# Kernel tuning notes

Hardware: AMD Instinct MI355X
Metric: run time of the kernel (lower is better)

The kernel has to match this reference:

```python
import jax, jax.numpy as jnp
import numpy as np
import math

B, T, C, H = 2, 2048, 1024, 16
D = C // H  # head dim 64

def setup_inputs() -> dict:
    key = jax.random.key(0)
    ks = jax.random.split(key, 3)
    scale = 0.02
    return {
        "x": jax.random.normal(ks[0], (B, T, C), dtype=jnp.float32),
        "W_attn": jax.random.normal(ks[1], (C, 3 * C), dtype=jnp.float32) * scale,
        "b_attn": jnp.zeros((3 * C,), dtype=jnp.float32),
        "W_proj": jax.random.normal(ks[2], (C, C), dtype=jnp.float32) * scale,
        "b_proj": jnp.zeros((C,), dtype=jnp.float32),
    }

def reference(x, W_attn, b_attn, W_proj, b_proj):
    Bb, Tt, Cc = x.shape
    qkv = x @ W_attn + b_attn                       # [B,T,3C]
    q, k, v = jnp.split(qkv, 3, axis=-1)
    # [B,T,C] -> [B,H,T,D]
    def heads(t):
        return t.reshape(Bb, Tt, H, D).transpose(0, 2, 1, 3)
    q, k, v = heads(q), heads(k), heads(v)
    scores = jnp.einsum('bhqd,bhkd->bhqk', q, k) * (1.0 / math.sqrt(D))
    causal = jnp.tril(jnp.ones((Tt, Tt), dtype=bool))
    scores = jnp.where(causal, scores, -jnp.inf)
    attn = jax.nn.softmax(scores, axis=-1)
    out = jnp.einsum('bhqk,bhkd->bhqd', attn, v)    # [B,H,T,D]
    out = out.transpose(0, 2, 1, 3).reshape(Bb, Tt, Cc)
    return out @ W_proj + b_proj
```

## Files before the change

kernel.cpp:

```cpp
#include <hip/hip_runtime.h>

typedef unsigned short u16;
typedef unsigned int u32;
typedef float f32x4 __attribute__((ext_vector_type(4)));
typedef float f32x16 __attribute__((ext_vector_type(16)));
typedef unsigned int u32x4 __attribute__((ext_vector_type(4)));
typedef unsigned int u32x2 __attribute__((ext_vector_type(2)));
typedef unsigned short u16x8 __attribute__((ext_vector_type(8)));
typedef unsigned short u16x4 __attribute__((ext_vector_type(4)));

#define DEV static __device__ __forceinline__

constexpr int BB = 2, TT = 2048, CC = 1024, HH = 16, DD = 64;
constexpr int MDIM = BB * TT;

DEV u16 f2bf(float f) {
  unsigned int u = __builtin_bit_cast(unsigned int, f);
  u += 0x7fffu + ((u >> 16) & 1u);
  return (u16)(u >> 16);
}
DEV float bf2f(u16 h) {
  unsigned int u = ((unsigned int)h) << 16;
  return __builtin_bit_cast(float, u);
}
DEV void async16(const void* g, void* l) {
  __builtin_amdgcn_global_load_lds(
      (const __attribute__((address_space(1))) unsigned int*)g,
      (__attribute__((address_space(3))) unsigned int*)l, 16, 0, 0);
}
DEV void mfma16(f32x4& acc, u32x4 a, u32x4 b) {
  asm volatile("v_mfma_f32_16x16x32_bf16 %0, %1, %2, %0"
               : "+v"(acc)
               : "v"(a), "v"(b));
}
DEV void mfma32(f32x16& acc, u32x4 a, u32x4 b) {
  asm volatile("v_mfma_f32_32x32x16_bf16 %0, %1, %2, %0"
               : "+v"(acc)
               : "v"(a), "v"(b));
}
DEV u32 cvtpk(float lo, float hi) {
  u32 r;
  asm("v_cvt_pk_bf16_f32 %0, %1, %2" : "=v"(r) : "v"(lo), "v"(hi));
  return r;
}
DEV void pswap(u32& a, u32& b) {
#if __has_builtin(__builtin_amdgcn_permlane32_swap)
  u32x2 r = __builtin_amdgcn_permlane32_swap(a, b, false, false);
  a = r.x;
  b = r.y;
#else
  asm volatile("v_permlane32_swap_b32 %0, %1" : "+v"(a), "+v"(b));
#endif
}
DEV float exp2g(float x) {
#if __has_builtin(__builtin_amdgcn_exp2f)
  return __builtin_amdgcn_exp2f(x);
#else
  return exp2f(x);
#endif
}

__global__ void cvt_f32_bf16(const float* __restrict__ in, u16* __restrict__ out, int n) {
  const int i = (blockIdx.x * blockDim.x + threadIdx.x) * 4;
  if (i < n) {
    f32x4 v = *(const f32x4*)(in + i);
    u16x4 o;
#pragma unroll
    for (int j = 0; j < 4; ++j) o[j] = f2bf(v[j]);
    *(u16x4*)(out + i) = o;
  }
}

__global__ void transpose_both(const float* __restrict__ Wa, const float* __restrict__ Wp,
                               u16* __restrict__ Wa_t, u16* __restrict__ Wp_t) {
  __shared__ float tile[32][33];
  int bx = blockIdx.x;
  const float* in;
  u16* out;
  int Cc;
  if (bx < 96) { in = Wa; out = Wa_t; Cc = 3072; }
  else { bx -= 96; in = Wp; out = Wp_t; Cc = 1024; }
  const int R = 1024;
  const int x0 = bx * 32, y0 = blockIdx.y * 32;
  const int tx = threadIdx.x, ty = threadIdx.y;
  tile[ty][tx] = in[(size_t)(y0 + ty) * Cc + (x0 + tx)];
  __syncthreads();
  out[(size_t)(x0 + ty) * R + (y0 + tx)] = f2bf(tile[tx][ty]);
}

template <int MODE>
__global__ __launch_bounds__(256) void gemm_bf16(
    const u16* __restrict__ A, const u16* __restrict__ Bt,
    const float* __restrict__ bias, float* __restrict__ outF,
    u16* __restrict__ qw, u16* __restrict__ kw, u16* __restrict__ vw,
    int M, int N, int K) {
  __shared__ alignas(16) u16 Sh[2][128 * 64];
  u16* Asp = Sh[0];
  u16* Bsp = Sh[1];
  const int tid = threadIdx.x;
  const int lane = tid & 63, w = tid >> 6;
  const int g = lane >> 4, c16 = lane & 15;
  const int wm = (w >> 1) * 64, wn = (w & 1) * 64;
  const int brow = blockIdx.y * 128, bcol = blockIdx.x * 128;
  const int lrow = lane >> 3;
  const int scol = ((lane & 7) ^ lrow) << 4;
  const int rswz = (c16 & 7) << 4;

  f32x4 acc[4][4];
#pragma unroll
  for (int m = 0; m < 4; ++m)
#pragma unroll
    for (int n = 0; n < 4; ++n) acc[m][n] = f32x4{0.f, 0.f, 0.f, 0.f};

  const size_t ldb = (size_t)K * 2;
  const char* Abase = (const char*)A + (size_t)brow * ldb;
  const char* Bbase = (const char*)Bt + (size_t)bcol * ldb;

  for (int kt = 0; kt < K; kt += 64) {
    __syncthreads();
#pragma unroll
    for (int i = 0; i < 4; ++i) {
      const int chunk = i * 4 + w;
      const int row = chunk * 8 + lrow;
      async16(Abase + (size_t)row * ldb + (size_t)kt * 2 + scol, (char*)Asp + chunk * 1024);
      async16(Bbase + (size_t)row * ldb + (size_t)kt * 2 + scol, (char*)Bsp + chunk * 1024);
    }
    __syncthreads();
#pragma unroll
    for (int kc = 0; kc < 2; ++kc) {
      const int cb = (kc * 64 + g * 16) ^ rswz;
      u32x4 af[4], bf8[4];
#pragma unroll
      for (int m = 0; m < 4; ++m)
        af[m] = *(const u32x4*)((const char*)Asp + (wm + m * 16 + c16) * 128 + cb);
#pragma unroll
      for (int n = 0; n < 4; ++n)
        bf8[n] = *(const u32x4*)((const char*)Bsp + (wn + n * 16 + c16) * 128 + cb);
#pragma unroll
      for (int m = 0; m < 4; ++m)
#pragma unroll
        for (int n = 0; n < 4; ++n) mfma16(acc[m][n], af[m], bf8[n]);
    }
  }

  if (MODE == 0) {
    float* Ef = (float*)&Sh[0][0];
#pragma unroll
    for (int pass = 0; pass < 2; ++pass) {
      __syncthreads();
      if ((wm >> 6) == pass) {
#pragma unroll
        for (int n = 0; n < 4; ++n) {
          const float bv = bias[bcol + wn + n * 16 + c16];
#pragma unroll
          for (int m = 0; m < 4; ++m)
#pragma unroll
            for (int r = 0; r < 4; ++r)
              Ef[(m * 16 + g * 4 + r) * 128 + wn + n * 16 + c16] = acc[m][n][r] + bv;
        }
      }
      __syncthreads();
#pragma unroll
      for (int i = 0; i < 8; ++i) {
        const int chunk = tid + i * 256;
        const int row = chunk >> 5;
        const int c4 = (chunk & 31) * 4;
        f32x4 v4 = *(const f32x4*)&Ef[row * 128 + c4];
        *(f32x4*)&outF[(size_t)(brow + pass * 64 + row) * N + bcol + c4] = v4;
      }
    }
  } else {
    u16* E = &Sh[0][0];
    const int which = bcol >> 10;
    __syncthreads();
    if (which < 2) {
#pragma unroll
      for (int n = 0; n < 4; ++n) {
        const float bv = bias[bcol + wn + n * 16 + c16];
#pragma unroll
        for (int m = 0; m < 4; ++m)
#pragma unroll
          for (int r = 0; r < 4; ++r)
            E[(wm + m * 16 + g * 4 + r) * 128 + wn + n * 16 + c16] =
                f2bf(acc[m][n][r] + bv);
      }
    } else {
#pragma unroll
      for (int n = 0; n < 4; ++n) {
        const float bv = bias[bcol + wn + n * 16 + c16];
#pragma unroll
        for (int m = 0; m < 4; ++m) {
          u16x4 t4;
#pragma unroll
          for (int r = 0; r < 4; ++r) t4[r] = f2bf(acc[m][n][r] + bv);
          *(u16x4*)&E[(wn + n * 16 + c16) * 128 + wm + m * 16 + g * 4] = t4;
        }
      }
    }
    __syncthreads();
#pragma unroll
    for (int i = 0; i < 8; ++i) {
      const int chunk = tid + i * 256;
      if (which < 2) {
        const int row = chunk >> 4;
        const int cc8 = (chunk & 15) * 8;
        const int colg = bcol + cc8;
        const int c = colg & 1023, h = c >> 6, d = c & 63;
        const int rowg = brow + row, b = rowg >> 11, t = rowg & (TT - 1);
        u16x8 v8 = *(const u16x8*)&E[row * 128 + cc8];
        u16* dst = (which == 0 ? qw : kw) + ((size_t)(b * HH + h) * TT + t) * DD + d;
        *(u16x8*)dst = v8;
      } else {
        const int drow = chunk >> 4;
        const int t8 = (chunk & 15) * 8;
        const int colg = bcol + drow;
        const int c = colg & 1023, h = c >> 6, d = c & 63;
        const int rowg = brow + t8, b = rowg >> 11, t = rowg & (TT - 1);
        u16x8 v8 = *(const u16x8*)&E[drow * 128 + t8];
        u16* dst = vw + ((size_t)(b * HH + h) * DD + d) * TT + t;
        *(u16x8*)dst = v8;
      }
    }
  }
}

__global__ __launch_bounds__(256) void attn_fwd(
    const u16* __restrict__ qw, const u16* __restrict__ kw,
    const u16* __restrict__ vw, u16* __restrict__ ao) {
  __shared__ alignas(16) u16 Ks[3][64 * 64];
  __shared__ alignas(16) u16 Vs[3][64 * 64];
  const int tid = threadIdx.x;
  const int lane = tid & 63, w = tid >> 6;
  const int ql = lane & 31, half = lane >> 5;
  const int bh = blockIdx.y;
  const int qb = ((bh >> 4) & 1) ? (15 - blockIdx.x) : blockIdx.x;
  const int q0w = qb * 128 + w * 32;
  const int qg = q0w + ql;
  const int lrow = lane >> 3;
  const int scol = ((lane & 7) ^ lrow) << 4;
  const int rswz = (ql & 7) << 4;

  u32x4 qf[4];
  {
    const u16* qrow = qw + ((size_t)bh * TT + qg) * DD;
    const float qs = 0.125f * 1.44269504f;
#pragma unroll
    for (int dwin = 0; dwin < 4; ++dwin) {
      u16x8 u = *(const u16x8*)(qrow + dwin * 16 + half * 8);
      u16x8 s;
#pragma unroll
      for (int j = 0; j < 8; ++j) s[j] = f2bf(bf2f(u[j]) * qs);
      qf[dwin] = __builtin_bit_cast(u32x4, s);
    }
  }

  f32x16 o0, o1;
#pragma unroll
  for (int i = 0; i < 16; ++i) { o0[i] = 0.f; o1[i] = 0.f; }
  float m_run = -1e30f, l_run = 0.f;

  const char* kbase = (const char*)kw + ((size_t)bh * TT) * 128;
  const char* vbase = (const char*)vw + ((size_t)bh * DD) * (TT * 2);

  const int nt = 2 * qb + 2;

#define STAGE(buf, kt_)                                                           \
  do {                                                                            \
    const int t0_ = (kt_)*64;                                                     \
    _Pragma("unroll") for (int i_ = 0; i_ < 2; ++i_) {                            \
      const int chunk_ = w * 2 + i_;                                              \
      const int row_ = chunk_ * 8 + lrow;                                         \
      async16(kbase + (size_t)(t0_ + row_) * 128 + scol,                          \
              (char*)Ks[buf] + chunk_ * 1024);                                    \
      async16(vbase + (size_t)row_ * (TT * 2) + (size_t)t0_ * 2 + scol,           \
              (char*)Vs[buf] + chunk_ * 1024);                                    \
    }                                                                             \
  } while (0)

  STAGE(0, 0);
  if (nt > 1) STAGE(1, 1);
  int rbuf = 0, sbuf = 2;

  for (int kt = 0; kt < nt; ++kt) {
    if (kt + 1 < nt)
      asm volatile("s_waitcnt vmcnt(4)" ::: "memory");
    else
      asm volatile("s_waitcnt vmcnt(0)" ::: "memory");
    __builtin_amdgcn_sched_barrier(0);
    __builtin_amdgcn_s_barrier();
    __builtin_amdgcn_sched_barrier(0);
    if (kt + 2 < nt) STAGE(sbuf, kt + 2);

    const int t0 = kt * 64;
    const char* Kc = (const char*)Ks[rbuf];
    const char* Vc = (const char*)Vs[rbuf];

    if (t0 < q0w + 32) {
      f32x16 s0, s1;
#pragma unroll
      for (int i = 0; i < 16; ++i) { s0[i] = 0.f; s1[i] = 0.f; }
      __builtin_amdgcn_s_setprio(1);
#pragma unroll
      for (int dwin = 0; dwin < 4; ++dwin) {
        const int cb = (dwin * 32 + half * 16) ^ rswz;
        u32x4 ak0 = *(const u32x4*)(Kc + (0 + ql) * 128 + cb);
        u32x4 ak1 = *(const u32x4*)(Kc + (32 + ql) * 128 + cb);
        mfma32(s0, ak0, qf[dwin]);
        mfma32(s1, ak1, qf[dwin]);
      }
      __builtin_amdgcn_s_setprio(0);

      if (t0 + 63 > q0w) {
        const int kb = t0 + 4 * half - qg;
#pragma unroll
        for (int r = 0; r < 16; ++r) {
          const int ko = (r & 3) + 8 * (r >> 2);
          if (kb + ko > 0) s0[r] = -1e30f;
          if (kb + 32 + ko > 0) s1[r] = -1e30f;
        }
      }

      float m8[8];
#pragma unroll
      for (int i = 0; i < 8; ++i)
        m8[i] = fmaxf(fmaxf(s0[i], s0[i + 8]), fmaxf(s1[i], s1[i + 8]));
      float mx = fmaxf(fmaxf(fmaxf(m8[0], m8[1]), fmaxf(m8[2], m8[3])),
                       fmaxf(fmaxf(m8[4], m8[5]), fmaxf(m8[6], m8[7])));
      mx = fmaxf(mx, __shfl_xor(mx, 32, 64));
      if (!__all(mx <= m_run + 8.f)) {
        const float mnew = fmaxf(m_run, mx);
        const float corr = exp2g(m_run - mnew);
        m_run = mnew;
        l_run *= corr;
#pragma unroll
        for (int i = 0; i < 16; ++i) { o0[i] *= corr; o1[i] *= corr; }
      }
#pragma unroll
      for (int i = 0; i < 16; ++i) {
        s0[i] = exp2g(s0[i] - m_run);
        s1[i] = exp2g(s1[i] - m_run);
      }
      float a8[8];
#pragma unroll
      for (int i = 0; i < 8; ++i)
        a8[i] = (s0[i] + s0[i + 8]) + (s1[i] + s1[i + 8]);
      float rs = ((a8[0] + a8[1]) + (a8[2] + a8[3])) + ((a8[4] + a8[5]) + (a8[6] + a8[7]));
      rs += __shfl_xor(rs, 32, 64);
      l_run += rs;

      u32x4 pf[4];
#pragma unroll
      for (int win = 0; win < 4; ++win) {
        const int b = (win & 1) * 8;
        u32 w0, w1, w2, w3;
        if (win < 2) {
          w0 = cvtpk(s0[b + 0], s0[b + 1]); w2 = cvtpk(s0[b + 4], s0[b + 5]);
          w1 = cvtpk(s0[b + 2], s0[b + 3]); w3 = cvtpk(s0[b + 6], s0[b + 7]);
        } else {
          w0 = cvtpk(s1[b + 0], s1[b + 1]); w2 = cvtpk(s1[b + 4], s1[b + 5]);
          w1 = cvtpk(s1[b + 2], s1[b + 3]); w3 = cvtpk(s1[b + 6], s1[b + 7]);
        }
        pswap(w0, w2);
        pswap(w1, w3);
        pf[win] = u32x4{w0, w1, w2, w3};
      }

      __builtin_amdgcn_s_setprio(1);
#pragma unroll
      for (int win = 0; win < 4; ++win) {
        const int cb = (win * 32 + half * 16) ^ rswz;
        u32x4 av0 = *(const u32x4*)(Vc + (0 + ql) * 128 + cb);
        u32x4 av1 = *(const u32x4*)(Vc + (32 + ql) * 128 + cb);
        mfma32(o0, av0, pf[win]);
        mfma32(o1, av1, pf[win]);
      }
      __builtin_amdgcn_s_setprio(0);
    }

    rbuf = (rbuf == 2) ? 0 : rbuf + 1;
    sbuf = (sbuf == 2) ? 0 : sbuf + 1;
  }
#undef STAGE

  const int b = bh >> 4, h = bh & 15;
  const float inv = 1.f / l_run;
  u16* aorow = ao + ((size_t)(b * TT) + qg) * CC + h * DD;
#pragma unroll
  for (int rg = 0; rg < 4; ++rg) {
    u16x4 t0v, t1v;
#pragma unroll
    for (int j = 0; j < 4; ++j) {
      t0v[j] = f2bf(o0[rg * 4 + j] * inv);
      t1v[j] = f2bf(o1[rg * 4 + j] * inv);
    }
    *(u16x4*)(aorow + 8 * rg + 4 * half) = t0v;
    *(u16x4*)(aorow + 32 + 8 * rg + 4 * half) = t1v;
  }
}

extern "C" void kernel_launch(void* const* d_in, const int* in_sizes, int n_in,
                              void* d_out, int out_size, void* d_ws, size_t ws_size,
                              hipStream_t stream) {
  const float* x  = (const float*)d_in[0];
  const float* Wa = (const float*)d_in[1];
  const float* ba = (const float*)d_in[2];
  const float* Wp = (const float*)d_in[3];
  const float* bp = (const float*)d_in[4];
  float* out = (float*)d_out;

  char* ws = (char*)d_ws;
  const size_t MB = 1ull << 20;
  u16* x_bf = (u16*)(ws);
  u16* ao   = (u16*)(ws);
  u16* Wa_t = (u16*)(ws + 8 * MB);
  u16* Wp_t = (u16*)(ws + 14 * MB);
  u16* q_ws = (u16*)(ws + 16 * MB);
  u16* k_ws = (u16*)(ws + 24 * MB);
  u16* v_ws = (u16*)(ws + 32 * MB);

  hipLaunchKernelGGL(cvt_f32_bf16, dim3((MDIM * CC) / 1024), dim3(256), 0, stream,
                     x, x_bf, MDIM * CC);
  hipLaunchKernelGGL(transpose_both, dim3(128, 32), dim3(32, 32), 0, stream,
                     Wa, Wp, Wa_t, Wp_t);
  hipLaunchKernelGGL((gemm_bf16<1>), dim3(3 * CC / 128, MDIM / 128), dim3(256), 0, stream,
                     x_bf, Wa_t, ba, nullptr, q_ws, k_ws, v_ws, MDIM, 3 * CC, CC);
  hipLaunchKernelGGL(attn_fwd, dim3(TT / 128, BB * HH), dim3(256), 0, stream,
                     q_ws, k_ws, v_ws, ao);
  hipLaunchKernelGGL((gemm_bf16<0>), dim3(CC / 128, MDIM / 128), dim3(256), 0, stream,
                     ao, Wp_t, bp, out, nullptr, nullptr, nullptr, MDIM, CC, CC);
}
```

Before: 124.7 us.

## Load K/V tiles directly from global memory per wave, dropping LDS pipeline

The attention kernel no longer stages K and V tiles through a triple-buffered shared-memory pipeline with async copies and block barriers. Each wave now reads its K and V fragments straight from global memory into registers and loops only over its own causal tile count. This removes barrier synchronisation and LDS traffic and lets each wave stop at its own causal limit. The cost is that the four waves of a block each fetch the same K/V data separately from cache, prefetching across iterations is lost, and register pressure rises.

After: 138.7 us. 11.2% more time.

```diff
diff --git a/kernel.cpp b/kernel.cpp
--- a/kernel.cpp
+++ b/kernel.cpp
@@ -227,8 +227,6 @@
 __global__ __launch_bounds__(256) void attn_fwd(
     const u16* __restrict__ qw, const u16* __restrict__ kw,
     const u16* __restrict__ vw, u16* __restrict__ ao) {
-  __shared__ alignas(16) u16 Ks[3][64 * 64];
-  __shared__ alignas(16) u16 Vs[3][64 * 64];
   const int tid = threadIdx.x;
   const int lane = tid & 63, w = tid >> 6;
   const int ql = lane & 31, half = lane >> 5;
@@ -236,9 +234,6 @@
   const int qb = ((bh >> 4) & 1) ? (15 - blockIdx.x) : blockIdx.x;
   const int q0w = qb * 128 + w * 32;
   const int qg = q0w + ql;
-  const int lrow = lane >> 3;
-  const int scol = ((lane & 7) ^ lrow) << 4;
-  const int rswz = (ql & 7) << 4;
 
   u32x4 qf[4];
   {
@@ -262,125 +257,99 @@
   const char* kbase = (const char*)kw + ((size_t)bh * TT) * 128;
   const char* vbase = (const char*)vw + ((size_t)bh * DD) * (TT * 2);
 
-  const int nt = 2 * qb + 2;
-
-#define STAGE(buf, kt_)                                                           \
-  do {                                                                            \
-    const int t0_ = (kt_)*64;                                                     \
-    _Pragma("unroll") for (int i_ = 0; i_ < 2; ++i_) {                            \
-      const int chunk_ = w * 2 + i_;                                              \
-      const int row_ = chunk_ * 8 + lrow;                                         \
-      async16(kbase + (size_t)(t0_ + row_) * 128 + scol,                          \
-              (char*)Ks[buf] + chunk_ * 1024);                                    \
-      async16(vbase + (size_t)row_ * (TT * 2) + (size_t)t0_ * 2 + scol,           \
-              (char*)Vs[buf] + chunk_ * 1024);                                    \
-    }                                                                             \
-  } while (0)
-
-  STAGE(0, 0);
-  if (nt > 1) STAGE(1, 1);
-  int rbuf = 0, sbuf = 2;
-
-  for (int kt = 0; kt < nt; ++kt) {
-    if (kt + 1 < nt)
-      asm volatile("s_waitcnt vmcnt(4)" ::: "memory");
-    else
-      asm volatile("s_waitcnt vmcnt(0)" ::: "memory");
-    __builtin_amdgcn_sched_barrier(0);
-    __builtin_amdgcn_s_barrier();
-    __builtin_amdgcn_sched_barrier(0);
-    if (kt + 2 < nt) STAGE(sbuf, kt + 2);
-
+  const int ntw = (q0w + 95) / 64;
+
+  for (int kt = 0; kt < ntw; ++kt) {
     const int t0 = kt * 64;
-    const char* Kc = (const char*)Ks[rbuf];
-    const char* Vc = (const char*)Vs[rbuf];
-
-    if (t0 < q0w + 32) {
-      f32x16 s0, s1;
-#pragma unroll
-      for (int i = 0; i < 16; ++i) { s0[i] = 0.f; s1[i] = 0.f; }
-      __builtin_amdgcn_s_setprio(1);
-#pragma unroll
-      for (int dwin = 0; dwin < 4; ++dwin) {
-        const int cb = (dwin * 32 + half * 16) ^ rswz;
-        u32x4 ak0 = *(const u32x4*)(Kc + (0 + ql) * 128 + cb);
-        u32x4 ak1 = *(const u32x4*)(Kc + (32 + ql) * 128 + cb);
-        mfma32(s0, ak0, qf[dwin]);
-        mfma32(s1, ak1, qf[dwin]);
-      }
-      __builtin_amdgcn_s_setprio(0);
-
-      if (t0 + 63 > q0w) {
-        const int kb = t0 + 4 * half - qg;
-#pragma unroll
-        for (int r = 0; r < 16; ++r) {
-          const int ko = (r & 3) + 8 * (r >> 2);
-          if (kb + ko > 0) s0[r] = -1e30f;
-          if (kb + 32 + ko > 0) s1[r] = -1e30f;
-        }
-      }
-
-      float m8[8];
-#pragma unroll
-      for (int i = 0; i < 8; ++i)
-        m8[i] = fmaxf(fmaxf(s0[i], s0[i + 8]), fmaxf(s1[i], s1[i + 8]));
-      float mx = fmaxf(fmaxf(fmaxf(m8[0], m8[1]), fmaxf(m8[2], m8[3])),
-                       fmaxf(fmaxf(m8[4], m8[5]), fmaxf(m8[6], m8[7])));
-      mx = fmaxf(mx, __shfl_xor(mx, 32, 64));
-      if (!__all(mx <= m_run + 8.f)) {
-        const float mnew = fmaxf(m_run, mx);
-        const float corr = exp2g(m_run - mnew);
-        m_run = mnew;
-        l_run *= corr;
-#pragma unroll
-        for (int i = 0; i < 16; ++i) { o0[i] *= corr; o1[i] *= corr; }
-      }
-#pragma unroll
-      for (int i = 0; i < 16; ++i) {
-        s0[i] = exp2g(s0[i] - m_run);
-        s1[i] = exp2g(s1[i] - m_run);
-      }
-      float a8[8];
-#pragma unroll
-      for (int i = 0; i < 8; ++i)
-        a8[i] = (s0[i] + s0[i + 8]) + (s1[i] + s1[i + 8]);
-      float rs = ((a8[0] + a8[1]) + (a8[2] + a8[3])) + ((a8[4] + a8[5]) + (a8[6] + a8[7]));
-      rs += __shfl_xor(rs, 32, 64);
-      l_run += rs;
-
-      u32x4 pf[4];
-#pragma unroll
-      for (int win = 0; win < 4; ++win) {
-        const int b = (win & 1) * 8;
-        u32 w0, w1, w2, w3;
-        if (win < 2) {
-          w0 = cvtpk(s0[b + 0], s0[b + 1]); w2 = cvtpk(s0[b + 4], s0[b + 5]);
-          w1 = cvtpk(s0[b + 2], s0[b + 3]); w3 = cvtpk(s0[b + 6], s0[b + 7]);
-        } else {
-          w0 = cvtpk(s1[b + 0], s1[b + 1]); w2 = cvtpk(s1[b + 4], s1[b + 5]);
-          w1 = cvtpk(s1[b + 2], s1[b + 3]); w3 = cvtpk(s1[b + 6], s1[b + 7]);
-        }
-        pswap(w0, w2);
-        pswap(w1, w3);
-        pf[win] = u32x4{w0, w1, w2, w3};
-      }
-
-      __builtin_amdgcn_s_setprio(1);
-#pragma unroll
-      for (int win = 0; win < 4; ++win) {
-        const int cb = (win * 32 + half * 16) ^ rswz;
-        u32x4 av0 = *(const u32x4*)(Vc + (0 + ql) * 128 + cb);
-        u32x4 av1 = *(const u32x4*)(Vc + (32 + ql) * 128 + cb);
-        mfma32(o0, av0, pf[win]);
-        mfma32(o1, av1, pf[win]);
-      }
-      __builtin_amdgcn_s_setprio(0);
-    }
-
-    rbuf = (rbuf == 2) ? 0 : rbuf + 1;
-    sbuf = (sbuf == 2) ? 0 : sbuf + 1;
-  }
-#undef STAGE
+    const char* Kt = kbase + (size_t)t0 * 128;
+
+    u32x4 ak[8];
+#pragma unroll
+    for (int dwin = 0; dwin < 4; ++dwin) {
+      ak[dwin]     = *(const u32x4*)(Kt + (0 + ql) * 128 + dwin * 32 + half * 16);
+      ak[dwin + 4] = *(const u32x4*)(Kt + (32 + ql) * 128 + dwin * 32 + half * 16);
+    }
+    u32x4 av[8];
+#pragma unroll
+    for (int win = 0; win < 4; ++win) {
+      av[win]     = *(const u32x4*)(vbase + (size_t)(0 + ql) * (TT * 2) + t0 * 2 + win * 32 + half * 16);
+      av[win + 4] = *(const u32x4*)(vbase + (size_t)(32 + ql) * (TT * 2) + t0 * 2 + win * 32 + half * 16);
+    }
+
+    f32x16 s0, s1;
+#pragma unroll
+    for (int i = 0; i < 16; ++i) { s0[i] = 0.f; s1[i] = 0.f; }
+    __builtin_amdgcn_s_setprio(1);
+#pragma unroll
+    for (int dwin = 0; dwin < 4; ++dwin) {
+      mfma32(s0, ak[dwin], qf[dwin]);
+      mfma32(s1, ak[dwin + 4], qf[dwin]);
+    }
+    __builtin_amdgcn_s_setprio(0);
+
+    if (t0 + 63 > q0w) {
+      const int kb = t0 + 4 * half - qg;
+#pragma unroll
+      for (int r = 0; r < 16; ++r) {
+        const int ko = (r & 3) + 8 * (r >> 2);
+        if (kb + ko > 0) s0[r] = -1e30f;
+        if (kb + 32 + ko > 0) s1[r] = -1e30f;
+      }
+    }
+
+    float m8[8];
+#pragma unroll
+    for (int i = 0; i < 8; ++i)
+      m8[i] = fmaxf(fmaxf(s0[i], s0[i + 8]), fmaxf(s1[i], s1[i + 8]));
+    float mx = fmaxf(fmaxf(fmaxf(m8[0], m8[1]), fmaxf(m8[2], m8[3])),
+                     fmaxf(fmaxf(m8[4], m8[5]), fmaxf(m8[6], m8[7])));
+    mx = fmaxf(mx, __shfl_xor(mx, 32, 64));
+    if (!__all(mx <= m_run + 8.f)) {
+      const float mnew = fmaxf(m_run, mx);
+      const float corr = exp2g(m_run - mnew);
+      m_run = mnew;
+      l_run *= corr;
+#pragma unroll
+      for (int i = 0; i < 16; ++i) { o0[i] *= corr; o1[i] *= corr; }
+    }
+#pragma unroll
+    for (int i = 0; i < 16; ++i) {
+      s0[i] = exp2g(s0[i] - m_run);
+      s1[i] = exp2g(s1[i] - m_run);
+    }
+    float a8[8];
+#pragma unroll
+    for (int i = 0; i < 8; ++i)
+      a8[i] = (s0[i] + s0[i + 8]) + (s1[i] + s1[i + 8]);
+    float rs = ((a8[0] + a8[1]) + (a8[2] + a8[3])) + ((a8[4] + a8[5]) + (a8[6] + a8[7]));
+    rs += __shfl_xor(rs, 32, 64);
+    l_run += rs;
+
+    u32x4 pf[4];
+#pragma unroll
+    for (int win = 0; win < 4; ++win) {
+      const int b = (win & 1) * 8;
+      u32 w0, w1, w2, w3;
+      if (win < 2) {
+        w0 = cvtpk(s0[b + 0], s0[b + 1]); w2 = cvtpk(s0[b + 4], s0[b + 5]);
+        w1 = cvtpk(s0[b + 2], s0[b + 3]); w3 = cvtpk(s0[b + 6], s0[b + 7]);
+      } else {
+        w0 = cvtpk(s1[b + 0], s1[b + 1]); w2 = cvtpk(s1[b + 4], s1[b + 5]);
+        w1 = cvtpk(s1[b + 2], s1[b + 3]); w3 = cvtpk(s1[b + 6], s1[b + 7]);
+      }
+      pswap(w0, w2);
+      pswap(w1, w3);
+      pf[win] = u32x4{w0, w1, w2, w3};
+    }
+
+    __builtin_amdgcn_s_setprio(1);
+#pragma unroll
+    for (int win = 0; win < 4; ++win) {
+      mfma32(o0, av[win], pf[win]);
+      mfma32(o1, av[win + 4], pf[win]);
+    }
+    __builtin_amdgcn_s_setprio(0);
+  }
 
   const int b = bh >> 4, h = bh & 15;
   const float inv = 1.f / l_run;
```

## Double-buffer GEMM k-loop and use 64-row tiles for output projection

Applied to the files above, without the earlier changes.

The bf16 GEMM now keeps two shared-memory buffers in dynamic LDS and issues the async loads for the next k-tile before computing on the current one. This overlaps global-to-LDS copies with MFMA work and leaves one barrier per iteration instead of two. The output-projection GEMM is templated to use 64-row M tiles, which doubles its grid to 512 blocks to improve CU occupancy. The cost is more LDS per block (64 KB and 48 KB), which may cut the number of resident blocks per CU.

New measurement: 145.7 us. 1.17x slower.

```diff
diff --git a/kernel.cpp b/kernel.cpp
--- a/kernel.cpp
+++ b/kernel.cpp
@@ -88,27 +88,30 @@
   out[(size_t)(x0 + ty) * R + (y0 + tx)] = f2bf(tile[tx][ty]);
 }
 
-template <int MODE>
+template <int MODE, int BM>
 __global__ __launch_bounds__(256) void gemm_bf16(
     const u16* __restrict__ A, const u16* __restrict__ Bt,
     const float* __restrict__ bias, float* __restrict__ outF,
     u16* __restrict__ qw, u16* __restrict__ kw, u16* __restrict__ vw,
     int M, int N, int K) {
-  __shared__ alignas(16) u16 Sh[2][128 * 64];
-  u16* Asp = Sh[0];
-  u16* Bsp = Sh[1];
+  extern __shared__ char smem_raw[];
+  u16* smem = (u16*)smem_raw;
+  u16* AsB[2] = {smem, smem + BM * 64};
+  u16* BsB[2] = {smem + 2 * BM * 64, smem + 2 * BM * 64 + 128 * 64};
+
   const int tid = threadIdx.x;
   const int lane = tid & 63, w = tid >> 6;
   const int g = lane >> 4, c16 = lane & 15;
-  const int wm = (w >> 1) * 64, wn = (w & 1) * 64;
-  const int brow = blockIdx.y * 128, bcol = blockIdx.x * 128;
+  const int wm = (w >> 1) * (BM / 2), wn = (w & 1) * 64;
+  const int brow = blockIdx.y * BM, bcol = blockIdx.x * 128;
   const int lrow = lane >> 3;
   const int scol = ((lane & 7) ^ lrow) << 4;
   const int rswz = (c16 & 7) << 4;
-
-  f32x4 acc[4][4];
-#pragma unroll
-  for (int m = 0; m < 4; ++m)
+  constexpr int MF = BM / 32;
+
+  f32x4 acc[MF][4];
+#pragma unroll
+  for (int m = 0; m < MF; ++m)
 #pragma unroll
     for (int n = 0; n < 4; ++n) acc[m][n] = f32x4{0.f, 0.f, 0.f, 0.f};
 
@@ -116,69 +119,85 @@
   const char* Abase = (const char*)A + (size_t)brow * ldb;
   const char* Bbase = (const char*)Bt + (size_t)bcol * ldb;
 
-  for (int kt = 0; kt < K; kt += 64) {
-    __syncthreads();
+  auto STAGE = [&](int buf, int kt_) {
+    const size_t ko = (size_t)kt_ * 128;
+#pragma unroll
+    for (int i = 0; i < BM / 32; ++i) {
+      const int chunk = w * (BM / 32) + i;
+      const int row = chunk * 8 + lrow;
+      async16(Abase + (size_t)row * ldb + ko + scol, (char*)AsB[buf] + chunk * 1024);
+    }
 #pragma unroll
     for (int i = 0; i < 4; ++i) {
-      const int chunk = i * 4 + w;
+      const int chunk = w * 4 + i;
       const int row = chunk * 8 + lrow;
-      async16(Abase + (size_t)row * ldb + (size_t)kt * 2 + scol, (char*)Asp + chunk * 1024);
-      async16(Bbase + (size_t)row * ldb + (size_t)kt * 2 + scol, (char*)Bsp + chunk * 1024);
-    }
-    __syncthreads();
+      async16(Bbase + (size_t)row * ldb + ko + scol, (char*)BsB[buf] + chunk * 1024);
+    }
+  };
+
+  const int NT = K / 64;
+  STAGE(0, 0);
+  asm volatile("s_waitcnt vmcnt(0)" ::: "memory");
+  __builtin_amdgcn_sched_barrier(0);
+  __builtin_amdgcn_s_barrier();
+
+  int cur = 0;
+  for (int kt = 0; kt < NT; ++kt) {
+    if (kt + 1 < NT) STAGE(cur ^ 1, kt + 1);
+    const char* Ap = (const char*)AsB[cur];
+    const char* Bp = (const char*)BsB[cur];
+    __builtin_amdgcn_s_setprio(1);
 #pragma unroll
     for (int kc = 0; kc < 2; ++kc) {
       const int cb = (kc * 64 + g * 16) ^ rswz;
-      u32x4 af[4], bf8[4];
-#pragma unroll
-      for (int m = 0; m < 4; ++m)
-        af[m] = *(const u32x4*)((const char*)Asp + (wm + m * 16 + c16) * 128 + cb);
+      u32x4 af[MF], bf8[4];
+#pragma unroll
+      for (int m = 0; m < MF; ++m)
+        af[m] = *(const u32x4*)(Ap + (wm + m * 16 + c16) * 128 + cb);
 #pragma unroll
       for (int n = 0; n < 4; ++n)
-        bf8[n] = *(const u32x4*)((const char*)Bsp + (wn + n * 16 + c16) * 128 + cb);
-#pragma unroll
-      for (int m = 0; m < 4; ++m)
+        bf8[n] = *(const u32x4*)(Bp + (wn + n * 16 + c16) * 128 + cb);
+#pragma unroll
+      for (int m = 0; m < MF; ++m)
 #pragma unroll
         for (int n = 0; n < 4; ++n) mfma16(acc[m][n], af[m], bf8[n]);
     }
+    __builtin_amdgcn_s_setprio(0);
+    asm volatile("s_waitcnt vmcnt(0)" ::: "memory");
+    __builtin_amdgcn_sched_barrier(0);
+    __builtin_amdgcn_s_barrier();
+    cur ^= 1;
   }
 
   if (MODE == 0) {
-    float* Ef = (float*)&Sh[0][0];
-#pragma unroll
-    for (int pass = 0; pass < 2; ++pass) {
-      __syncthreads();
-      if ((wm >> 6) == pass) {
-#pragma unroll
-        for (int n = 0; n < 4; ++n) {
-          const float bv = bias[bcol + wn + n * 16 + c16];
-#pragma unroll
-          for (int m = 0; m < 4; ++m)
-#pragma unroll
-            for (int r = 0; r < 4; ++r)
-              Ef[(m * 16 + g * 4 + r) * 128 + wn + n * 16 + c16] = acc[m][n][r] + bv;
-        }
-      }
-      __syncthreads();
-#pragma unroll
-      for (int i = 0; i < 8; ++i) {
-        const int chunk = tid + i * 256;
-        const int row = chunk >> 5;
-        const int c4 = (chunk & 31) * 4;
-        f32x4 v4 = *(const f32x4*)&Ef[row * 128 + c4];
-        *(f32x4*)&outF[(size_t)(brow + pass * 64 + row) * N + bcol + c4] = v4;
-      }
+    float* Ef = (float*)smem;
+#pragma unroll
+    for (int n = 0; n < 4; ++n) {
+      const float bv = bias[bcol + wn + n * 16 + c16];
+#pragma unroll
+      for (int m = 0; m < MF; ++m)
+#pragma unroll
+        for (int r = 0; r < 4; ++r)
+          Ef[(wm + m * 16 + g * 4 + r) * 128 + wn + n * 16 + c16] = acc[m][n][r] + bv;
+    }
+    __syncthreads();
+#pragma unroll
+    for (int i = 0; i < 8; ++i) {
+      const int chunk = tid + i * 256;
+      const int row = chunk >> 5;
+      const int c4 = (chunk & 31) * 4;
+      f32x4 v4 = *(const f32x4*)&Ef[row * 128 + c4];
+      *(f32x4*)&outF[(size_t)(brow + row) * N + bcol + c4] = v4;
     }
   } else {
-    u16* E = &Sh[0][0];
+    u16* E = smem;
     const int which = bcol >> 10;
-    __syncthreads();
     if (which < 2) {
 #pragma unroll
       for (int n = 0; n < 4; ++n) {
         const float bv = bias[bcol + wn + n * 16 + c16];
 #pragma unroll
-        for (int m = 0; m < 4; ++m)
+        for (int m = 0; m < MF; ++m)
 #pragma unroll
           for (int r = 0; r < 4; ++r)
             E[(wm + m * 16 + g * 4 + r) * 128 + wn + n * 16 + c16] =
@@ -189,7 +208,7 @@
       for (int n = 0; n < 4; ++n) {
         const float bv = bias[bcol + wn + n * 16 + c16];
 #pragma unroll
-        for (int m = 0; m < 4; ++m) {
+        for (int m = 0; m < MF; ++m) {
           u16x4 t4;
 #pragma unroll
           for (int r = 0; r < 4; ++r) t4[r] = f2bf(acc[m][n][r] + bv);
@@ -264,7 +283,7 @@
 
   const int nt = 2 * qb + 2;
 
-#define STAGE(buf, kt_)                                                           \
+#define STAGE_AT(buf, kt_)                                                        \
   do {                                                                            \
     const int t0_ = (kt_)*64;                                                     \
     _Pragma("unroll") for (int i_ = 0; i_ < 2; ++i_) {                            \
@@ -277,8 +296,8 @@
     }                                                                             \
   } while (0)
 
-  STAGE(0, 0);
-  if (nt > 1) STAGE(1, 1);
+  STAGE_AT(0, 0);
+  if (nt > 1) STAGE_AT(1, 1);
   int rbuf = 0, sbuf = 2;
 
   for (int kt = 0; kt < nt; ++kt) {
@@ -289,7 +308,7 @@
     __builtin_amdgcn_sched_barrier(0);
     __builtin_amdgcn_s_barrier();
     __builtin_amdgcn_sched_barrier(0);
-    if (kt + 2 < nt) STAGE(sbuf, kt + 2);
+    if (kt + 2 < nt) STAGE_AT(sbuf, kt + 2);
 
     const int t0 = kt * 64;
     const char* Kc = (const char*)Ks[rbuf];
@@ -380,7 +399,7 @@
     rbuf = (rbuf == 2) ? 0 : rbuf + 1;
     sbuf = (sbuf == 2) ? 0 : sbuf + 1;
   }
-#undef STAGE
+#undef STAGE_AT
 
   const int b = bh >> 4, h = bh & 15;
   const float inv = 1.f / l_run;
@@ -422,10 +441,12 @@
                      x, x_bf, MDIM * CC);
   hipLaunchKernelGGL(transpose_both, dim3(128, 32), dim3(32, 32), 0, stream,
                      Wa, Wp, Wa_t, Wp_t);
-  hipLaunchKernelGGL((gemm_bf16<1>), dim3(3 * CC / 128, MDIM / 128), dim3(256), 0, stream,
+  hipLaunchKernelGGL((gemm_bf16<1, 128>), dim3(3 * CC / 128, MDIM / 128), dim3(256),
+                     65536, stream,
                      x_bf, Wa_t, ba, nullptr, q_ws, k_ws, v_ws, MDIM, 3 * CC, CC);
   hipLaunchKernelGGL(attn_fwd, dim3(TT / 128, BB * HH), dim3(256), 0, stream,
                      q_ws, k_ws, v_ws, ao);
-  hipLaunchKernelGGL((gemm_bf16<0>), dim3(CC / 128, MDIM / 128), dim3(256), 0, stream,
+  hipLaunchKernelGGL((gemm_bf16<0, 64>), dim3(CC / 128, MDIM / 64), dim3(256),
+                     49152, stream,
                      ao, Wp_t, bp, out, nullptr, nullptr, nullptr, MDIM, CC, CC);
 }
```

## Software-pipeline attention QK of next tile with softmax and PV of current tile

Applied to the files above, without the earlier changes.

The attention loop is restructured so the QK^T MFMAs for tile kt+1 are issued before the masking, softmax and PV work of tile kt, with two sets of score registers alternating between tiles. The K/V shared-memory ring grows from three to four stages in 64KB of dynamic LDS, and prefetch now runs three tiles ahead. The aim is to hide exp and reduction latency behind matrix-core work and to keep loads further in flight. In exchange it raises register pressure and LDS use per block, which may cut the number of resident blocks per CU.

New measurement: 119.8 us (median of 2 runs). -4.0%, faster.

```diff
diff --git a/kernel.cpp b/kernel.cpp
--- a/kernel.cpp
+++ b/kernel.cpp
@@ -227,8 +227,7 @@
 __global__ __launch_bounds__(256) void attn_fwd(
     const u16* __restrict__ qw, const u16* __restrict__ kw,
     const u16* __restrict__ vw, u16* __restrict__ ao) {
-  __shared__ alignas(16) u16 Ks[3][64 * 64];
-  __shared__ alignas(16) u16 Vs[3][64 * 64];
+  extern __shared__ u16 smem[];
   const int tid = threadIdx.x;
   const int lane = tid & 63, w = tid >> 6;
   const int ql = lane & 31, half = lane >> 5;
@@ -264,123 +263,142 @@
 
   const int nt = 2 * qb + 2;
 
-#define STAGE(buf, kt_)                                                           \
-  do {                                                                            \
-    const int t0_ = (kt_)*64;                                                     \
-    _Pragma("unroll") for (int i_ = 0; i_ < 2; ++i_) {                            \
-      const int chunk_ = w * 2 + i_;                                              \
-      const int row_ = chunk_ * 8 + lrow;                                         \
-      async16(kbase + (size_t)(t0_ + row_) * 128 + scol,                          \
-              (char*)Ks[buf] + chunk_ * 1024);                                    \
-      async16(vbase + (size_t)row_ * (TT * 2) + (size_t)t0_ * 2 + scol,           \
-              (char*)Vs[buf] + chunk_ * 1024);                                    \
-    }                                                                             \
-  } while (0)
-
-  STAGE(0, 0);
-  if (nt > 1) STAGE(1, 1);
-  int rbuf = 0, sbuf = 2;
-
-  for (int kt = 0; kt < nt; ++kt) {
-    if (kt + 1 < nt)
-      asm volatile("s_waitcnt vmcnt(4)" ::: "memory");
-    else
-      asm volatile("s_waitcnt vmcnt(0)" ::: "memory");
-    __builtin_amdgcn_sched_barrier(0);
-    __builtin_amdgcn_s_barrier();
-    __builtin_amdgcn_sched_barrier(0);
-    if (kt + 2 < nt) STAGE(sbuf, kt + 2);
-
-    const int t0 = kt * 64;
-    const char* Kc = (const char*)Ks[rbuf];
-    const char* Vc = (const char*)Vs[rbuf];
-
-    if (t0 < q0w + 32) {
-      f32x16 s0, s1;
-#pragma unroll
-      for (int i = 0; i < 16; ++i) { s0[i] = 0.f; s1[i] = 0.f; }
-      __builtin_amdgcn_s_setprio(1);
-#pragma unroll
-      for (int dwin = 0; dwin < 4; ++dwin) {
-        const int cb = (dwin * 32 + half * 16) ^ rswz;
-        u32x4 ak0 = *(const u32x4*)(Kc + (0 + ql) * 128 + cb);
-        u32x4 ak1 = *(const u32x4*)(Kc + (32 + ql) * 128 + cb);
-        mfma32(s0, ak0, qf[dwin]);
-        mfma32(s1, ak1, qf[dwin]);
-      }
-      __builtin_amdgcn_s_setprio(0);
-
-      if (t0 + 63 > q0w) {
-        const int kb = t0 + 4 * half - qg;
-#pragma unroll
-        for (int r = 0; r < 16; ++r) {
-          const int ko = (r & 3) + 8 * (r >> 2);
-          if (kb + ko > 0) s0[r] = -1e30f;
-          if (kb + 32 + ko > 0) s1[r] = -1e30f;
-        }
-      }
-
-      float m8[8];
-#pragma unroll
-      for (int i = 0; i < 8; ++i)
-        m8[i] = fmaxf(fmaxf(s0[i], s0[i + 8]), fmaxf(s1[i], s1[i + 8]));
-      float mx = fmaxf(fmaxf(fmaxf(m8[0], m8[1]), fmaxf(m8[2], m8[3])),
-                       fmaxf(fmaxf(m8[4], m8[5]), fmaxf(m8[6], m8[7])));
-      mx = fmaxf(mx, __shfl_xor(mx, 32, 64));
-      if (!__all(mx <= m_run + 8.f)) {
-        const float mnew = fmaxf(m_run, mx);
-        const float corr = exp2g(m_run - mnew);
-        m_run = mnew;
-        l_run *= corr;
-#pragma unroll
-        for (int i = 0; i < 16; ++i) { o0[i] *= corr; o1[i] *= corr; }
-      }
-#pragma unroll
-      for (int i = 0; i < 16; ++i) {
-        s0[i] = exp2g(s0[i] - m_run);
-        s1[i] = exp2g(s1[i] - m_run);
-      }
-      float a8[8];
-#pragma unroll
-      for (int i = 0; i < 8; ++i)
-        a8[i] = (s0[i] + s0[i + 8]) + (s1[i] + s1[i + 8]);
-      float rs = ((a8[0] + a8[1]) + (a8[2] + a8[3])) + ((a8[4] + a8[5]) + (a8[6] + a8[7]));
-      rs += __shfl_xor(rs, 32, 64);
-      l_run += rs;
-
-      u32x4 pf[4];
-#pragma unroll
-      for (int win = 0; win < 4; ++win) {
-        const int b = (win & 1) * 8;
-        u32 w0, w1, w2, w3;
-        if (win < 2) {
-          w0 = cvtpk(s0[b + 0], s0[b + 1]); w2 = cvtpk(s0[b + 4], s0[b + 5]);
-          w1 = cvtpk(s0[b + 2], s0[b + 3]); w3 = cvtpk(s0[b + 6], s0[b + 7]);
-        } else {
-          w0 = cvtpk(s1[b + 0], s1[b + 1]); w2 = cvtpk(s1[b + 4], s1[b + 5]);
-          w1 = cvtpk(s1[b + 2], s1[b + 3]); w3 = cvtpk(s1[b + 6], s1[b + 7]);
-        }
-        pswap(w0, w2);
-        pswap(w1, w3);
-        pf[win] = u32x4{w0, w1, w2, w3};
-      }
-
-      __builtin_amdgcn_s_setprio(1);
-#pragma unroll
-      for (int win = 0; win < 4; ++win) {
-        const int cb = (win * 32 + half * 16) ^ rswz;
-        u32x4 av0 = *(const u32x4*)(Vc + (0 + ql) * 128 + cb);
-        u32x4 av1 = *(const u32x4*)(Vc + (32 + ql) * 128 + cb);
-        mfma32(o0, av0, pf[win]);
-        mfma32(o1, av1, pf[win]);
-      }
-      __builtin_amdgcn_s_setprio(0);
-    }
-
-    rbuf = (rbuf == 2) ? 0 : rbuf + 1;
-    sbuf = (sbuf == 2) ? 0 : sbuf + 1;
-  }
-#undef STAGE
+  auto kptr = [&](int b) { return (char*)(smem + b * 4096); };
+  auto vptr = [&](int b) { return (char*)(smem + 16384 + b * 4096); };
+
+  auto STAGE = [&](int kt_) {
+    if (kt_ >= nt) return;
+    const int buf = kt_ & 3;
+    const int t0_ = kt_ * 64;
+#pragma unroll
+    for (int i_ = 0; i_ < 2; ++i_) {
+      const int chunk = w * 2 + i_;
+      const int row = chunk * 8 + lrow;
+      async16(kbase + (size_t)(t0_ + row) * 128 + scol, kptr(buf) + chunk * 1024);
+      async16(vbase + (size_t)row * (TT * 2) + (size_t)t0_ * 2 + scol,
+              vptr(buf) + chunk * 1024);
+    }
+  };
+
+  auto QK = [&](int kt_, f32x16& sa, f32x16& sb) {
+    const char* Kc = kptr(kt_ & 3);
+#pragma unroll
+    for (int i = 0; i < 16; ++i) { sa[i] = 0.f; sb[i] = 0.f; }
+    __builtin_amdgcn_s_setprio(1);
+#pragma unroll
+    for (int dwin = 0; dwin < 4; ++dwin) {
+      const int cb = (dwin * 32 + half * 16) ^ rswz;
+      u32x4 ak0 = *(const u32x4*)(Kc + (0 + ql) * 128 + cb);
+      u32x4 ak1 = *(const u32x4*)(Kc + (32 + ql) * 128 + cb);
+      mfma32(sa, ak0, qf[dwin]);
+      mfma32(sb, ak1, qf[dwin]);
+    }
+    __builtin_amdgcn_s_setprio(0);
+  };
+
+  auto FINISH = [&](int kt_, f32x16& s0, f32x16& s1) {
+    const int t0 = kt_ * 64;
+    if (t0 >= q0w + 32) return;
+    if (t0 + 63 > q0w) {
+      const int kb = t0 + 4 * half - qg;
+#pragma unroll
+      for (int r = 0; r < 16; ++r) {
+        const int ko = (r & 3) + 8 * (r >> 2);
+        if (kb + ko > 0) s0[r] = -1e30f;
+        if (kb + 32 + ko > 0) s1[r] = -1e30f;
+      }
+    }
+    float m8[8];
+#pragma unroll
+    for (int i = 0; i < 8; ++i)
+      m8[i] = fmaxf(fmaxf(s0[i], s0[i + 8]), fmaxf(s1[i], s1[i + 8]));
+    float mx = fmaxf(fmaxf(fmaxf(m8[0], m8[1]), fmaxf(m8[2], m8[3])),
+                     fmaxf(fmaxf(m8[4], m8[5]), fmaxf(m8[6], m8[7])));
+    mx = fmaxf(mx, __shfl_xor(mx, 32, 64));
+    if (!__all(mx <= m_run + 8.f)) {
+      const float mnew = fmaxf(m_run, mx);
+      const float corr = exp2g(m_run - mnew);
+      m_run = mnew;
+      l_run *= corr;
+#pragma unroll
+      for (int i = 0; i < 16; ++i) { o0[i] *= corr; o1[i] *= corr; }
+    }
+#pragma unroll
+    for (int i = 0; i < 16; ++i) {
+      s0[i] = exp2g(s0[i] - m_run);
+      s1[i] = exp2g(s1[i] - m_run);
+    }
+    float a8[8];
+#pragma unroll
+    for (int i = 0; i < 8; ++i)
+      a8[i] = (s0[i] + s0[i + 8]) + (s1[i] + s1[i + 8]);
+    float rs = ((a8[0] + a8[1]) + (a8[2] + a8[3])) + ((a8[4] + a8[5]) + (a8[6] + a8[7]));
+    rs += __shfl_xor(rs, 32, 64);
+    l_run += rs;
+
+    u32x4 pf[4];
+#pragma unroll
+    for (int win = 0; win < 4; ++win) {
+      const int b = (win & 1) * 8;
+      u32 w0, w1, w2, w3;
+      if (win < 2) {
+        w0 = cvtpk(s0[b + 0], s0[b + 1]); w2 = cvtpk(s0[b + 4], s0[b + 5]);
+        w1 = cvtpk(s0[b + 2], s0[b + 3]); w3 = cvtpk(s0[b + 6], s0[b + 7]);
+      } else {
+        w0 = cvtpk(s1[b + 0], s1[b + 1]); w2 = cvtpk(s1[b + 4], s1[b + 5]);
+        w1 = cvtpk(s1[b + 2], s1[b + 3]); w3 = cvtpk(s1[b + 6], s1[b + 7]);
+      }
+      pswap(w0, w2);
+      pswap(w1, w3);
+      pf[win] = u32x4{w0, w1, w2, w3};
+    }
+    const char* Vc = vptr(kt_ & 3);
+    __builtin_amdgcn_s_setprio(1);
+#pragma unroll
+    for (int win = 0; win < 4; ++win) {
+      const int cb = (win * 32 + half * 16) ^ rswz;
+      u32x4 av0 = *(const u32x4*)(Vc + (0 + ql) * 128 + cb);
+      u32x4 av1 = *(const u32x4*)(Vc + (32 + ql) * 128 + cb);
+      mfma32(o0, av0, pf[win]);
+      mfma32(o1, av1, pf[win]);
+    }
+    __builtin_amdgcn_s_setprio(0);
+  };
+
+  STAGE(0);
+  STAGE(1);
+  STAGE(2);
+  if (nt >= 3)
+    asm volatile("s_waitcnt vmcnt(8)" ::: "memory");
+  else
+    asm volatile("s_waitcnt vmcnt(4)" ::: "memory");
+  __builtin_amdgcn_sched_barrier(0);
+  __builtin_amdgcn_s_barrier();
+  __builtin_amdgcn_sched_barrier(0);
+
+  f32x16 sA0, sA1, sB0, sB1;
+  QK(0, sA0, sA1);
+
+#define BODY(KT, C0, C1, N0, N1)                                          \
+  {                                                                       \
+    const int kt_b = (KT);                                                \
+    if (kt_b + 2 < nt)                                                    \
+      asm volatile("s_waitcnt vmcnt(4)" ::: "memory");                    \
+    else                                                                  \
+      asm volatile("s_waitcnt vmcnt(0)" ::: "memory");                    \
+    __builtin_amdgcn_sched_barrier(0);                                    \
+    __builtin_amdgcn_s_barrier();                                         \
+    __builtin_amdgcn_sched_barrier(0);                                    \
+    STAGE(kt_b + 3);                                                      \
+    if (kt_b + 1 < nt && (kt_b + 1) * 64 < q0w + 32) QK(kt_b + 1, N0, N1);\
+    FINISH(kt_b, C0, C1);                                                 \
+  }
+
+  for (int kt2 = 0; kt2 < nt; kt2 += 2) {
+    BODY(kt2, sA0, sA1, sB0, sB1);
+    BODY(kt2 + 1, sB0, sB1, sA0, sA1);
+  }
+#undef BODY
 
   const int b = bh >> 4, h = bh & 15;
   const float inv = 1.f / l_run;
@@ -424,7 +442,7 @@
                      Wa, Wp, Wa_t, Wp_t);
   hipLaunchKernelGGL((gemm_bf16<1>), dim3(3 * CC / 128, MDIM / 128), dim3(256), 0, stream,
                      x_bf, Wa_t, ba, nullptr, q_ws, k_ws, v_ws, MDIM, 3 * CC, CC);
-  hipLaunchKernelGGL(attn_fwd, dim3(TT / 128, BB * HH), dim3(256), 0, stream,
+  hipLaunchKernelGGL(attn_fwd, dim3(TT / 128, BB * HH), dim3(256), 65536, stream,
                      q_ws, k_ws, v_ws, ao);
   hipLaunchKernelGGL((gemm_bf16<0>), dim3(CC / 128, MDIM / 128), dim3(256), 0, stream,
                      ao, Wp_t, bp, out, nullptr, nullptr, nullptr, MDIM, CC, CC);
```
